# Kernel tuning notes

Measured on AMD Instinct MI355X. Metric: run time of the kernel, lower is better.

## Reference

```python
import jax, jax.numpy as jnp
import numpy as np

EPS = 1e-6

def _rmsnorm(x, g):
    return x * jax.lax.rsqrt(jnp.mean(x * x, axis=-1, keepdims=True) + EPS) * g

def _linear(x, w, b):
    # torch nn.Linear convention: w is [out, in]
    return jnp.einsum('bld,hd->blh', x, w) + b

def setup_inputs() -> dict:
    key = jax.random.key(0)
    ks = jax.random.split(key, 10)
    B, L, D, H = 4, 4096, 1024, 2048
    s = 0.02
    return {
        'x': jax.random.normal(ks[0], (B, L, D), jnp.float32),
        'hidden': jax.random.normal(ks[1], (B, H), jnp.float32),
        'w_forget': jax.random.normal(ks[2], (H, D), jnp.float32) * s,
        'b_forget': jnp.zeros((H,), jnp.float32),
        'w_input': jax.random.normal(ks[3], (H, D), jnp.float32) * s,
        'b_input': jnp.zeros((H,), jnp.float32),
        'w_hout': jax.random.normal(ks[4], (D, H), jnp.float32) * s,
        'b_hout': jnp.zeros((D,), jnp.float32),
        'w_fc': jax.random.normal(ks[5], (H, D), jnp.float32) * s,
        'b_fc': jnp.zeros((H,), jnp.float32),
        'w_fc_act': jax.random.normal(ks[6], (H, D), jnp.float32) * s,
        'b_fc_act': jnp.zeros((H,), jnp.float32),
        'w_fout': jax.random.normal(ks[7], (D, H), jnp.float32) * s,
        'b_fout': jnp.zeros((D,), jnp.float32),
        'g_norm1': jnp.ones((D,), jnp.float32),
        'g_norm2': jnp.ones((D,), jnp.float32),
    }

def reference(x, hidden, w_forget, b_forget, w_input, b_input, w_hout, b_hout,
              w_fc, b_fc, w_fc_act, b_fc_act, w_fout, b_fout, g_norm1, g_norm2):
    H = hidden.shape[-1]
    # --- QGRU sub-block (pre-norm residual) ---
    xr = x
    xn = _rmsnorm(x, g_norm1)
    decay = jnp.linspace(0.0, 1.0, H, dtype=x.dtype)  # [H]
    remember = jax.nn.sigmoid(_linear(xn, w_forget, b_forget)) * decay  # [B,L,H]
    forget = 1.0 - remember
    inp = jnp.tanh(_linear(xn, w_input, b_input))
    # inclusive linear recurrence h[t] = forget[t]*h[t-1] + remember[t]*inp[t]
    def combine(c1, c2):
        a1, b1 = c1
        a2, b2 = c2
        return (a2 * a1, a2 * b1 + b2)
    _, h_inner = jax.lax.associative_scan(combine, (forget, inp * remember), axis=1)
    # fold in initial hidden state: h = h_inner + hidden * cumprod(forget)
    h = h_inner + hidden[:, None, :] * jnp.cumprod(forget, axis=1)  # [B,L,H]
    y = jnp.einsum('blh,dh->bld', h, w_hout) + b_hout
    x1 = y + xr  # dropout is identity in eval
    # --- FFN SwiGLU sub-block (pre-norm residual) ---
    xn2 = _rmsnorm(x1, g_norm2)
    ff = _linear(xn2, w_fc, b_fc) * jax.nn.silu(_linear(xn2, w_fc_act, b_fc_act))
    out = jnp.einsum('blh,dh->bld', ff, w_fout) + b_fout + x1
    return (out, h[:, -1, :])
```

## Files before the change

### kernel.cpp

```cpp
#include <hip/hip_runtime.h>
#include <hip/hip_bf16.h>

typedef __bf16 bf16x8 __attribute__((ext_vector_type(8)));
typedef __bf16 bf16x4 __attribute__((ext_vector_type(4)));
typedef float floatx4 __attribute__((ext_vector_type(4)));

#define LFULL 4096

__device__ __forceinline__ void gll16(const __bf16* g, __bf16* l) {
    __builtin_amdgcn_global_load_lds(
        (const __attribute__((address_space(1))) void*)g,
        (__attribute__((address_space(3))) void*)l, 16, 0, 0);
}

template <int RD>
__global__ __launch_bounds__(512, 2) void gemm_bt(
    const __bf16* __restrict__ A, const __bf16* __restrict__ Bw,
    const float* __restrict__ bias, const void* __restrict__ Rp,
    void* __restrict__ Cp, int K, int N, int sT, int t0)
{
    __shared__ __align__(16) __bf16 As[4][256][32];
    __shared__ __align__(16) __bf16 Bs[4][256][32];

    const int tid  = threadIdx.x;

    const int nwg = gridDim.x * gridDim.y;
    int bid = blockIdx.y * gridDim.x + blockIdx.x;
    bid = (bid & 7) * (nwg >> 3) + (bid >> 3);
    const int m0 = (bid / gridDim.x) * 256;
    const int n0 = (bid % gridDim.x) * 256;

    const int wave = tid >> 6;
    const int lane = tid & 63;
    const int wm   = (wave & 1) * 128;
    const int wn   = (wave >> 1) * 64;
    const int q    = lane >> 4;
    const int ml   = lane & 15;
    const int ks   = (q ^ ((ml >> 1) & 3)) * 8;

    const int t8 = tid * 8;
    const int rA = tid >> 2;
    const int cg = ((tid & 3) ^ ((tid >> 3) & 3)) * 8;
    const __bf16* gA1 = A  + (size_t)(m0 + rA) * K + cg;
    const __bf16* gA2 = A  + (size_t)(m0 + 128 + rA) * K + cg;
    const __bf16* gB1 = Bw + (size_t)(n0 + rA) * K + cg;
    const __bf16* gB2 = Bw + (size_t)(n0 + 128 + rA) * K + cg;

    floatx4 acc[8][4] = {};
    int sb = 0;

#define STAGE_FULL() do { \
        __bf16* la = (__bf16*)As[sb & 3]; \
        __bf16* lb = (__bf16*)Bs[sb & 3]; \
        gll16(gA1, la + t8); \
        gll16(gA2, la + 4096 + t8); \
        gll16(gB1, lb + t8); \
        gll16(gB2, lb + 4096 + t8); \
        gA1 += 32; gA2 += 32; gB1 += 32; gB2 += 32; ++sb; \
    } while (0)

#define STAGE_A() do { \
        __bf16* la = (__bf16*)As[sb & 3]; \
        gll16(gA1, la + t8); \
        gll16(gA2, la + 4096 + t8); \
        gA1 += 32; gA2 += 32; \
    } while (0)

#define STAGE_B() do { \
        __bf16* lb = (__bf16*)Bs[sb & 3]; \
        gll16(gB1, lb + t8); \
        gll16(gB2, lb + 4096 + t8); \
        gB1 += 32; gB2 += 32; ++sb; \
    } while (0)

    const int NT = K >> 5;
    STAGE_FULL(); STAGE_FULL(); STAGE_FULL();
    asm volatile("s_waitcnt vmcnt(8)" ::: "memory");
    __builtin_amdgcn_s_barrier();

    for (int kt = 0; kt < NT; ++kt) {
        const int CB = kt & 3;
        const __bf16* Ab = &As[CB][0][0];
        const __bf16* Bb = &Bs[CB][0][0];
        bf16x8 af[4], bfr[4];
        const bool pre = (kt + 3 < NT);

#pragma unroll
        for (int i = 0; i < 4; i++)
            af[i] = *(const bf16x8*)(Ab + (wm + i * 16 + ml) * 32 + ks);
#pragma unroll
        for (int j = 0; j < 4; j++)
            bfr[j] = *(const bf16x8*)(Bb + (wn + j * 16 + ml) * 32 + ks);
        if (pre) STAGE_A();
        __builtin_amdgcn_s_barrier();
        asm volatile("s_waitcnt lgkmcnt(0)" ::: "memory");
        __builtin_amdgcn_sched_barrier(0);
        __builtin_amdgcn_s_setprio(1);
#pragma unroll
        for (int i = 0; i < 4; i++)
#pragma unroll
            for (int j = 0; j < 4; j++)
                acc[i][j] = __builtin_amdgcn_mfma_f32_16x16x32_bf16(af[i], bfr[j], acc[i][j], 0, 0, 0);
        __builtin_amdgcn_s_setprio(0);
        __builtin_amdgcn_s_barrier();

#pragma unroll
        for (int i = 0; i < 4; i++)
            af[i] = *(const bf16x8*)(Ab + (wm + 64 + i * 16 + ml) * 32 + ks);
        if (pre) STAGE_B();
        __builtin_amdgcn_s_barrier();
        asm volatile("s_waitcnt lgkmcnt(0)" ::: "memory");
        __builtin_amdgcn_sched_barrier(0);
        __builtin_amdgcn_s_setprio(1);
#pragma unroll
        for (int i = 0; i < 4; i++)
#pragma unroll
            for (int j = 0; j < 4; j++)
                acc[4 + i][j] = __builtin_amdgcn_mfma_f32_16x16x32_bf16(af[i], bfr[j], acc[4 + i][j], 0, 0, 0);
        __builtin_amdgcn_s_setprio(0);
        const int rem = NT - 1 - kt;
        if (rem >= 3)      { asm volatile("s_waitcnt vmcnt(8)" ::: "memory"); }
        else if (rem == 2) { asm volatile("s_waitcnt vmcnt(4)" ::: "memory"); }
        else if (rem == 1) { asm volatile("s_waitcnt vmcnt(0)" ::: "memory"); }
        __builtin_amdgcn_s_barrier();
    }

#undef STAGE_FULL
#undef STAGE_A
#undef STAGE_B

    const int Tmask = (1 << sT) - 1;
#pragma unroll
    for (int i = 0; i < 8; i++) {
#pragma unroll
        for (int j = 0; j < 4; j++) {
            const int n = n0 + wn + j * 16 + ml;
            const float bv = bias[n];
            const float dec = (float)n * (1.0f / 2047.0f);
#pragma unroll
            for (int r = 0; r < 4; r++) {
                const int m = m0 + wm + i * 16 + q * 4 + r;
                float v = acc[i][j][r] + bv;
                if (RD == 1) {
                    const int gm = ((m >> sT) * LFULL) + t0 + (m & Tmask);
                    v += ((const float*)Rp)[(size_t)gm * N + n];
                    ((__bf16*)Cp)[(size_t)m * N + n] = (__bf16)v;
                } else if (RD == 2) {
                    v += (float)((const __bf16*)Rp)[(size_t)m * N + n];
                    const int gm = ((m >> sT) * LFULL) + t0 + (m & Tmask);
                    ((float*)Cp)[(size_t)gm * N + n] = v;
                } else if (RD == 3) {
                    const float sl = v / (1.f + __expf(-v));
                    const float z1 = (float)((const __bf16*)Rp)[(size_t)m * N + n];
                    ((__bf16*)Cp)[(size_t)m * N + n] = (__bf16)(z1 * sl);
                } else if (RD == 4) {
                    const float rr = dec / (1.f + __expf(-v));
                    ((__bf16*)Cp)[(size_t)m * N + n] = (__bf16)rr;
                } else if (RD == 5) {
                    const float e = __expf(2.f * v);
                    const float th = 1.f - 2.f / (e + 1.f);
                    ((__bf16*)Cp)[(size_t)m * N + n] = (__bf16)th;
                } else {
                    ((__bf16*)Cp)[(size_t)m * N + n] = (__bf16)v;
                }
            }
        }
    }
}

__global__ __launch_bounds__(256) void cvt_w(
    const float* __restrict__ s0, const float* __restrict__ s1,
    const float* __restrict__ s2, const float* __restrict__ s3,
    const float* __restrict__ s4, const float* __restrict__ s5,
    __bf16* __restrict__ dst)
{
    const float* srcs[6] = {s0, s1, s2, s3, s4, s5};
    const float* s = srcs[blockIdx.y];
    __bf16* d = dst + (size_t)blockIdx.y * 2097152;
    const int i = (blockIdx.x * 256 + threadIdx.x) * 8;
    float4 f0 = *(const float4*)(s + i);
    float4 f1 = *(const float4*)(s + i + 4);
    bf16x8 o;
    o[0] = (__bf16)f0.x; o[1] = (__bf16)f0.y; o[2] = (__bf16)f0.z; o[3] = (__bf16)f0.w;
    o[4] = (__bf16)f1.x; o[5] = (__bf16)f1.y; o[6] = (__bf16)f1.z; o[7] = (__bf16)f1.w;
    *(bf16x8*)(d + i) = o;
}

__global__ __launch_bounds__(256) void rmsnorm_f32in(
    const float* __restrict__ x, const float* __restrict__ g,
    __bf16* __restrict__ o, int sT, int t0)
{
    const int r = blockIdx.x;
    const int grow = ((r >> sT) * LFULL) + t0 + (r & ((1 << sT) - 1));
    const float* xr = x + (size_t)grow * 1024;
    const int tid = threadIdx.x;

    float4 v = *(const float4*)(xr + tid * 4);
    float vv[4] = {v.x, v.y, v.z, v.w};
    float ss = vv[0] * vv[0] + vv[1] * vv[1] + vv[2] * vv[2] + vv[3] * vv[3];
#pragma unroll
    for (int off = 32; off > 0; off >>= 1) ss += __shfl_down(ss, off);

    __shared__ float red[4];
    if ((tid & 63) == 0) red[tid >> 6] = ss;
    __syncthreads();
    const float tot = red[0] + red[1] + red[2] + red[3];
    const float scale = rsqrtf(tot * (1.0f / 1024.0f) + 1e-6f);

    float4 g4 = *(const float4*)(g + tid * 4);
    float gg[4] = {g4.x, g4.y, g4.z, g4.w};
    bf16x4 ov;
#pragma unroll
    for (int e = 0; e < 4; e++) ov[e] = (__bf16)(vv[e] * scale * gg[e]);
    *(bf16x4*)(o + (size_t)r * 1024 + tid * 4) = ov;
}

__global__ __launch_bounds__(256) void rmsnorm_b16in(
    const __bf16* __restrict__ x, const float* __restrict__ g,
    __bf16* __restrict__ o)
{
    const int r = blockIdx.x;
    const __bf16* xr = x + (size_t)r * 1024;
    const int tid = threadIdx.x;

    bf16x4 v = *(const bf16x4*)(xr + tid * 4);
    float vv[4];
#pragma unroll
    for (int e = 0; e < 4; e++) vv[e] = (float)v[e];
    float ss = vv[0] * vv[0] + vv[1] * vv[1] + vv[2] * vv[2] + vv[3] * vv[3];
#pragma unroll
    for (int off = 32; off > 0; off >>= 1) ss += __shfl_down(ss, off);

    __shared__ float red[4];
    if ((tid & 63) == 0) red[tid >> 6] = ss;
    __syncthreads();
    const float tot = red[0] + red[1] + red[2] + red[3];
    const float scale = rsqrtf(tot * (1.0f / 1024.0f) + 1e-6f);

    float4 g4 = *(const float4*)(g + tid * 4);
    float gg[4] = {g4.x, g4.y, g4.z, g4.w};
    bf16x4 ov;
#pragma unroll
    for (int e = 0; e < 4; e++) ov[e] = (__bf16)(vv[e] * scale * gg[e]);
    *(bf16x4*)(o + (size_t)r * 1024 + tid * 4) = ov;
}

__global__ __launch_bounds__(256) void scan_pass1(
    const __bf16* __restrict__ rr, const __bf16* __restrict__ th,
    float* __restrict__ Ach, float* __restrict__ Bch, int T)
{
    const int h0 = threadIdx.x * 8;
    const int s = blockIdx.x;
    const int b = blockIdx.y;
    const int NSC = T >> 5;
    size_t p = ((size_t)b * T + s * 32) * 2048 + h0;
    float Aa[8], Bv[8];
#pragma unroll
    for (int e = 0; e < 8; e++) { Aa[e] = 1.f; Bv[e] = 0.f; }
    for (int t = 0; t < 32; t++, p += 2048) {
        bf16x8 rv = *(const bf16x8*)(rr + p);
        bf16x8 tv = *(const bf16x8*)(th + p);
#pragma unroll
        for (int e = 0; e < 8; e++) {
            const float r = (float)rv[e];
            const float a = 1.f - r;
            Aa[e] *= a;
            Bv[e] = a * Bv[e] + r * (float)tv[e];
        }
    }
    const size_t qq = (size_t)(b * NSC + s) * 2048 + h0;
#pragma unroll
    for (int e = 0; e < 8; e++) { Ach[qq + e] = Aa[e]; Bch[qq + e] = Bv[e]; }
}

__global__ __launch_bounds__(256) void scan_pass2(
    const float* __restrict__ Ach, const float* __restrict__ Bch,
    float* __restrict__ hst, const float* __restrict__ hidden,
    float* __restrict__ state, float* __restrict__ hlast,
    int NSC, int first, int last)
{
    const int idx = blockIdx.x * 256 + threadIdx.x;
    const int b = idx >> 11;
    const int h = idx & 2047;
    float hs = first ? hidden[idx] : state[idx];
    size_t qq = (size_t)b * NSC * 2048 + h;
#pragma unroll 4
    for (int s = 0; s < NSC; s++, qq += 2048) {
        hst[qq] = hs;
        hs = Ach[qq] * hs + Bch[qq];
    }
    state[idx] = hs;
    if (last) hlast[idx] = hs;
}

__global__ __launch_bounds__(256) void scan_pass3(
    __bf16* __restrict__ rio, const __bf16* __restrict__ th,
    const float* __restrict__ hst, int T)
{
    const int h0 = threadIdx.x * 8;
    const int s = blockIdx.x;
    const int b = blockIdx.y;
    const int NSC = T >> 5;
    float hp[8];
    const size_t qq = (size_t)(b * NSC + s) * 2048 + h0;
#pragma unroll
    for (int e = 0; e < 8; e++) hp[e] = hst[qq + e];
    size_t p = ((size_t)b * T + s * 32) * 2048 + h0;
    for (int t = 0; t < 32; t++, p += 2048) {
        bf16x8 rv = *(const bf16x8*)(rio + p);
        bf16x8 tv = *(const bf16x8*)(th + p);
        bf16x8 ov;
#pragma unroll
        for (int e = 0; e < 8; e++) {
            const float r = (float)rv[e];
            hp[e] = (1.f - r) * hp[e] + r * (float)tv[e];
            ov[e] = (__bf16)hp[e];
        }
        *(bf16x8*)(rio + p) = ov;
    }
}

extern "C" void kernel_launch(void* const* d_in, const int* in_sizes, int n_in,
                              void* d_out, int out_size, void* d_ws, size_t ws_size,
                              hipStream_t stream)
{
    const float* x        = (const float*)d_in[0];
    const float* hidden   = (const float*)d_in[1];
    const float* w_forget = (const float*)d_in[2];
    const float* b_forget = (const float*)d_in[3];
    const float* w_input  = (const float*)d_in[4];
    const float* b_input  = (const float*)d_in[5];
    const float* w_hout   = (const float*)d_in[6];
    const float* b_hout   = (const float*)d_in[7];
    const float* w_fc     = (const float*)d_in[8];
    const float* b_fc     = (const float*)d_in[9];
    const float* w_fc_act = (const float*)d_in[10];
    const float* b_fc_act = (const float*)d_in[11];
    const float* w_fout   = (const float*)d_in[12];
    const float* b_fout   = (const float*)d_in[13];
    const float* g_norm1  = (const float*)d_in[14];
    const float* g_norm2  = (const float*)d_in[15];

    float* out   = (float*)d_out;
    float* hlast = out + (size_t)16384 * 1024;

    int T = 4096;
    for (;;) {
        size_t need = 25165824ull + (size_t)4 * T * 12288 + 3ull * 4 * (T / 32) * 2048 * 4 + 65536;
        if (need <= ws_size || T == 256) break;
        T >>= 1;
    }
    const int NC = 4096 / T;
    int sT = 0; while ((1 << sT) < T) sT++;
    const int Mc = 4 * T;
    const int NSC = T >> 5;

    char* p = (char*)d_ws;
    __bf16* wb = (__bf16*)p; p += 25165824ull;
    __bf16* xn = (__bf16*)p; p += (size_t)Mc * 1024 * 2;
    __bf16* zf = (__bf16*)p; p += (size_t)Mc * 2048 * 2;
    __bf16* zi = (__bf16*)p; p += (size_t)Mc * 2048 * 2;
    __bf16* x1 = (__bf16*)p; p += (size_t)Mc * 1024 * 2;
    float* Ach = (float*)p;  p += (size_t)4 * NSC * 2048 * 4;
    float* Bch = (float*)p;  p += (size_t)4 * NSC * 2048 * 4;
    float* hst = (float*)p;  p += (size_t)4 * NSC * 2048 * 4;
    float* state = (float*)p;

    __bf16* wb_f  = wb;
    __bf16* wb_i  = wb + 2097152;
    __bf16* wb_fc = wb + 2 * 2097152;
    __bf16* wb_fa = wb + 3 * 2097152;
    __bf16* wb_h  = wb + 4 * 2097152;
    __bf16* wb_o  = wb + 5 * 2097152;

    cvt_w<<<dim3(1024, 6), 256, 0, stream>>>(w_forget, w_input, w_fc, w_fc_act, w_hout, w_fout, wb);

    for (int c = 0; c < NC; c++) {
        const int t0 = c * T;
        rmsnorm_f32in<<<Mc, 256, 0, stream>>>(x, g_norm1, xn, sT, t0);
        gemm_bt<4><<<dim3(8, Mc / 256), 512, 0, stream>>>(xn, wb_f, b_forget, nullptr, zf, 1024, 2048, sT, t0);
        gemm_bt<5><<<dim3(8, Mc / 256), 512, 0, stream>>>(xn, wb_i, b_input,  nullptr, zi, 1024, 2048, sT, t0);
        scan_pass1<<<dim3(NSC, 4), 256, 0, stream>>>(zf, zi, Ach, Bch, T);
        scan_pass2<<<32, 256, 0, stream>>>(Ach, Bch, hst, hidden, state, hlast, NSC,
                                           (c == 0) ? 1 : 0, (c == NC - 1) ? 1 : 0);
        scan_pass3<<<dim3(NSC, 4), 256, 0, stream>>>(zf, zi, hst, T);
        gemm_bt<1><<<dim3(4, Mc / 256), 512, 0, stream>>>(zf, wb_h, b_hout, x, x1, 2048, 1024, sT, t0);
        rmsnorm_b16in<<<Mc, 256, 0, stream>>>(x1, g_norm2, xn);
        gemm_bt<0><<<dim3(8, Mc / 256), 512, 0, stream>>>(xn, wb_fc, b_fc,     nullptr, zf, 1024, 2048, sT, t0);
        gemm_bt<3><<<dim3(8, Mc / 256), 512, 0, stream>>>(xn, wb_fa, b_fc_act, zf, zf, 1024, 2048, sT, t0);
        gemm_bt<2><<<dim3(4, Mc / 256), 512, 0, stream>>>(zf, wb_o, b_fout, x1, out, 2048, 1024, sT, t0);
    }
}
```

Baseline: 752.1 us.

## Replace 4-stage split A/B LDS pipeline with 2-stage double buffering in GEMM

Cuts the shared-memory ring from four stages to two and issues each tile's A and B loads together one tile ahead, waiting for all outstanding loads at the end of every iteration. It also reorders the MFMA loops so the B fragment index is outer. Halving LDS per block could allow more resident blocks, but prefetch distance drops from three tiles to one, so global load latency may be less well hidden.

```diff
diff --git a/kernel.cpp b/kernel.cpp
--- a/kernel.cpp
+++ b/kernel.cpp
@@ -19,8 +19,8 @@
     const float* __restrict__ bias, const void* __restrict__ Rp,
     void* __restrict__ Cp, int K, int N, int sT, int t0)
 {
-    __shared__ __align__(16) __bf16 As[4][256][32];
-    __shared__ __align__(16) __bf16 Bs[4][256][32];
+    __shared__ __align__(16) __bf16 As[2][256][32];
+    __shared__ __align__(16) __bf16 Bs[2][256][32];
 
     const int tid  = threadIdx.x;
 
@@ -49,9 +49,9 @@
     floatx4 acc[8][4] = {};
     int sb = 0;
 
-#define STAGE_FULL() do { \
-        __bf16* la = (__bf16*)As[sb & 3]; \
-        __bf16* lb = (__bf16*)Bs[sb & 3]; \
+#define STAGE() do { \
+        __bf16* la = (__bf16*)As[sb & 1]; \
+        __bf16* lb = (__bf16*)Bs[sb & 1]; \
         gll16(gA1, la + t8); \
         gll16(gA2, la + 4096 + t8); \
         gll16(gB1, lb + t8); \
@@ -59,31 +59,17 @@
         gA1 += 32; gA2 += 32; gB1 += 32; gB2 += 32; ++sb; \
     } while (0)
 
-#define STAGE_A() do { \
-        __bf16* la = (__bf16*)As[sb & 3]; \
-        gll16(gA1, la + t8); \
-        gll16(gA2, la + 4096 + t8); \
-        gA1 += 32; gA2 += 32; \
-    } while (0)
-
-#define STAGE_B() do { \
-        __bf16* lb = (__bf16*)Bs[sb & 3]; \
-        gll16(gB1, lb + t8); \
-        gll16(gB2, lb + 4096 + t8); \
-        gB1 += 32; gB2 += 32; ++sb; \
-    } while (0)
-
     const int NT = K >> 5;
-    STAGE_FULL(); STAGE_FULL(); STAGE_FULL();
-    asm volatile("s_waitcnt vmcnt(8)" ::: "memory");
+    STAGE();
+    asm volatile("s_waitcnt vmcnt(0)" ::: "memory");
     __builtin_amdgcn_s_barrier();
+    __builtin_amdgcn_sched_barrier(0);
 
     for (int kt = 0; kt < NT; ++kt) {
-        const int CB = kt & 3;
-        const __bf16* Ab = &As[CB][0][0];
-        const __bf16* Bb = &Bs[CB][0][0];
+        const __bf16* Ab = &As[kt & 1][0][0];
+        const __bf16* Bb = &Bs[kt & 1][0][0];
+        const bool more = (kt + 1 < NT);
         bf16x8 af[4], bfr[4];
-        const bool pre = (kt + 3 < NT);
 
 #pragma unroll
         for (int i = 0; i < 4; i++)
@@ -91,15 +77,15 @@
 #pragma unroll
         for (int j = 0; j < 4; j++)
             bfr[j] = *(const bf16x8*)(Bb + (wn + j * 16 + ml) * 32 + ks);
-        if (pre) STAGE_A();
+        if (more) STAGE();
         __builtin_amdgcn_s_barrier();
         asm volatile("s_waitcnt lgkmcnt(0)" ::: "memory");
         __builtin_amdgcn_sched_barrier(0);
         __builtin_amdgcn_s_setprio(1);
 #pragma unroll
-        for (int i = 0; i < 4; i++)
-#pragma unroll
-            for (int j = 0; j < 4; j++)
+        for (int j = 0; j < 4; j++)
+#pragma unroll
+            for (int i = 0; i < 4; i++)
                 acc[i][j] = __builtin_amdgcn_mfma_f32_16x16x32_bf16(af[i], bfr[j], acc[i][j], 0, 0, 0);
         __builtin_amdgcn_s_setprio(0);
         __builtin_amdgcn_s_barrier();
@@ -107,27 +93,24 @@
 #pragma unroll
         for (int i = 0; i < 4; i++)
             af[i] = *(const bf16x8*)(Ab + (wm + 64 + i * 16 + ml) * 32 + ks);
-        if (pre) STAGE_B();
         __builtin_amdgcn_s_barrier();
         asm volatile("s_waitcnt lgkmcnt(0)" ::: "memory");
         __builtin_amdgcn_sched_barrier(0);
         __builtin_amdgcn_s_setprio(1);
 #pragma unroll
-        for (int i = 0; i < 4; i++)
-#pragma unroll
-            for (int j = 0; j < 4; j++)
+        for (int j = 0; j < 4; j++)
+#pragma unroll
+            for (int i = 0; i < 4; i++)
                 acc[4 + i][j] = __builtin_amdgcn_mfma_f32_16x16x32_bf16(af[i], bfr[j], acc[4 + i][j], 0, 0, 0);
         __builtin_amdgcn_s_setprio(0);
-        const int rem = NT - 1 - kt;
-        if (rem >= 3)      { asm volatile("s_waitcnt vmcnt(8)" ::: "memory"); }
-        else if (rem == 2) { asm volatile("s_waitcnt vmcnt(4)" ::: "memory"); }
-        else if (rem == 1) { asm volatile("s_waitcnt vmcnt(0)" ::: "memory"); }
-        __builtin_amdgcn_s_barrier();
-    }
-
-#undef STAGE_FULL
-#undef STAGE_A
-#undef STAGE_B
+        if (more) {
+            asm volatile("s_waitcnt vmcnt(0)" ::: "memory");
+            __builtin_amdgcn_s_barrier();
+            __builtin_amdgcn_sched_barrier(0);
+        }
+    }
+
+#undef STAGE
 
     const int Tmask = (1 << sT) - 1;
 #pragma unroll
```

Result: slower. 806.8 us (+7.3%).
